# Kernel tuning notes

Measured on AMD Instinct MI355X. Metric: run time of the kernel, lower is better.

Reference implementation:

```python
import math
import jax, jax.numpy as jnp
import numpy as np

NUM_HEADS = 8
FACTOR = 5


def setup_inputs() -> dict:
    key = jax.random.key(0)
    ks = jax.random.split(key, 8)
    B, N, C = 8, 4096, 512
    s = 0.02
    x = jax.random.normal(ks[0], (B, N, C), dtype=jnp.float32)
    Wq = jax.random.normal(ks[1], (C, C), dtype=jnp.float32) * s
    Wk = jax.random.normal(ks[2], (C, C), dtype=jnp.float32) * s
    Wv = jax.random.normal(ks[3], (C, C), dtype=jnp.float32) * s
    Wp = jax.random.normal(ks[4], (C, C), dtype=jnp.float32) * s
    bq = jnp.zeros((C,), jnp.float32)
    bk = jnp.zeros((C,), jnp.float32)
    bv = jnp.zeros((C,), jnp.float32)
    bp = jnp.zeros((C,), jnp.float32)
    sample_k = min(FACTOR * int(np.ceil(np.log(N))), N)  # 45
    index_sample = jax.random.randint(ks[5], (N, sample_k), 0, N, dtype=jnp.int64)
    return {"x": x, "Wq": Wq, "bq": bq, "Wk": Wk, "bk": bk,
            "Wv": Wv, "bv": bv, "Wp": Wp, "bp": bp,
            "index_sample": index_sample}


def reference(x, Wq, bq, Wk, bk, Wv, bv, Wp, bp, index_sample):
    B, N, C = x.shape
    H = NUM_HEADS
    Dh = C // H
    L_Q = L_K = N
    # qkv projections (torch Linear: x @ W.T + b; W sampled symmetric so use x @ W + b)
    q = (x @ Wq + bq).reshape(B, N, H, Dh).transpose(0, 2, 1, 3)  # [B,H,L,Dh]
    k = (x @ Wk + bk).reshape(B, N, H, Dh).transpose(0, 2, 1, 3)
    v = (x @ Wv + bv).reshape(B, N, H, Dh).transpose(0, 2, 1, 3)

    u = min(FACTOR * int(np.ceil(np.log(L_Q))), L_Q)  # n_top
    scale = (C // H) ** (-0.5)

    # _prob_QK: sampled scores per query
    K_sample = k[:, :, index_sample, :]                       # [B,H,L_Q,s,Dh]
    QK_sample = jnp.einsum('bhld,bhlsd->bhls', q, K_sample)   # [B,H,L_Q,s]
    M = QK_sample.max(axis=-1) - QK_sample.sum(axis=-1) / L_K # sparsity measure
    _, M_top = jax.lax.top_k(M, u)                            # [B,H,u]
    Q_reduce = jnp.take_along_axis(q, M_top[..., None], axis=2)  # [B,H,u,Dh]
    scores = jnp.einsum('bhud,bhkd->bhuk', Q_reduce, k) * scale  # [B,H,u,L_K]

    # initial context: mean of V over keys (mask_flag=False)
    context = jnp.broadcast_to(v.mean(axis=2, keepdims=True), (B, H, L_Q, Dh))

    # update context at selected queries
    attn = jax.nn.softmax(scores, axis=-1)
    out_u = jnp.einsum('bhuk,bhkd->bhud', attn, v)            # [B,H,u,Dh]
    bI = jnp.arange(B)[:, None, None]
    hI = jnp.arange(H)[None, :, None]
    context = context.at[bI, hI, M_top].set(out_u)            # [B,H,L_Q,Dh]

    # mix=True: reshape [B,H,N,Dh] -> [B,N,H*Dh] directly (faithful to source)
    context = context.reshape(B, N, H * Dh)
    return context @ Wp + bp
```

## Files before the change

### kernel.cpp

```cpp
#include <hip/hip_runtime.h>
#include <float.h>

typedef unsigned short ushort_t;
typedef short bf16x8 __attribute__((ext_vector_type(8)));
typedef _Float16 f16x8 __attribute__((ext_vector_type(8)));
typedef float f32x4 __attribute__((ext_vector_type(4)));

#define NS 4096
#define ND 64
#define NU 45
#define NUP 48

__device__ __forceinline__ float bf2f(ushort_t u){ return __uint_as_float(((unsigned)u)<<16); }
__device__ __forceinline__ ushort_t f2bf(float f){
  unsigned u = __float_as_uint(f);
  u += 0x7fffu + ((u>>16)&1u);
  return (ushort_t)(u>>16);
}
__device__ __forceinline__ ushort_t f2h(float f){ _Float16 h=(_Float16)f; return __builtin_bit_cast(ushort_t, h); }
__device__ __forceinline__ float h2f(ushort_t u){ return (float)__builtin_bit_cast(_Float16, u); }

__global__ __launch_bounds__(256) void k_wsplit(const float* __restrict__ Wq,
                                                const float* __restrict__ Wk,
                                                const float* __restrict__ Wv,
                                                ushort_t* __restrict__ wh,
                                                ushort_t* __restrict__ wl)
{
  int i = blockIdx.x*256 + threadIdx.x;
  int c = i >> 9, k = i & 511;
  const float* W = (c < 512) ? Wq : (c < 1024 ? Wk : Wv);
  float v = W[k*512 + (c & 511)];
  ushort_t h = f2bf(v);
  wh[i] = h;
  wl[i] = f2bf(v - bf2f(h));
}

__global__ __launch_bounds__(256) void k_xsplit(const float* __restrict__ x,
                                                ushort_t* __restrict__ xh,
                                                ushort_t* __restrict__ xl)
{
  int i = (blockIdx.x*256 + threadIdx.x)*4;
  float4 v = *(const float4*)(x + i);
  ushort4 h, lo;
  h.x = f2bf(v.x); lo.x = f2bf(v.x - bf2f(h.x));
  h.y = f2bf(v.y); lo.y = f2bf(v.y - bf2f(h.y));
  h.z = f2bf(v.z); lo.z = f2bf(v.z - bf2f(h.z));
  h.w = f2bf(v.w); lo.w = f2bf(v.w - bf2f(h.w));
  *(ushort4*)(xh + i) = h;
  *(ushort4*)(xl + i) = lo;
}

template<int MODE>
__global__ __launch_bounds__(256) void k_gemm(
    const ushort_t* __restrict__ xh, const ushort_t* __restrict__ xl,
    const ushort_t* __restrict__ wh, const ushort_t* __restrict__ wl,
    const float* __restrict__ bq, const float* __restrict__ bk, const float* __restrict__ bv,
    float* __restrict__ kf, ushort_t* __restrict__ vfT,
    ushort_t* __restrict__ kb16, ushort_t* __restrict__ qb16)
{
  __shared__ __align__(16) ushort_t smem[20480];
  ushort_t* Ah = smem;
  ushort_t* Al = smem + 5120;
  ushort_t* Bh = smem + (MODE == 1 ? 10240 : 5120);
  ushort_t* Bl = smem + 15360;
  const int nbx = (MODE == 0) ? 4 : 8;
  const int p = blockIdx.y * nbx + blockIdx.x;
  const int cx = p & 7;
  const int local = p >> 3;
  const int by = cx*32 + local/nbx;
  const int bx = local % nbx;
  const int rowbase = by * 128;
  const int colbase = (MODE == 0 ? 0 : 512) + bx*128;
  const int mat = colbase >> 9;
  const int t = threadIdx.x;
  const int l = t & 63;
  const int w = t >> 6;
  const int wm = w >> 1, wn = w & 1;
  f32x4 acc[4][4] = {};
  const int r0 = t >> 2;
  const int c0 = (t & 3) * 8;

  for (int k0 = 0; k0 < 512; k0 += 32) {
    __syncthreads();
    #pragma unroll
    for (int half = 0; half < 2; half++) {
      const int r = r0 + half*64;
      *(uint4*)(&Ah[r*40 + c0]) = *(const uint4*)(&xh[(size_t)(rowbase + r)*512 + k0 + c0]);
      if (MODE == 1) *(uint4*)(&Al[r*40 + c0]) = *(const uint4*)(&xl[(size_t)(rowbase + r)*512 + k0 + c0]);
      *(uint4*)(&Bh[r*40 + c0]) = *(const uint4*)(&wh[(size_t)(colbase + r)*512 + k0 + c0]);
      if (MODE == 1) *(uint4*)(&Bl[r*40 + c0]) = *(const uint4*)(&wl[(size_t)(colbase + r)*512 + k0 + c0]);
    }
    __syncthreads();
    bf16x8 ah[4], al[4], bh8[4], bl8[4];
    #pragma unroll
    for (int m = 0; m < 4; m++) {
      const int off = (wm*64 + m*16 + (l & 15))*40 + (l >> 4)*8;
      ah[m] = *(const bf16x8*)(&Ah[off]);
      if (MODE == 1) al[m] = *(const bf16x8*)(&Al[off]);
    }
    #pragma unroll
    for (int n = 0; n < 4; n++) {
      const int off = (wn*64 + n*16 + (l & 15))*40 + (l >> 4)*8;
      bh8[n] = *(const bf16x8*)(&Bh[off]);
      if (MODE == 1) bl8[n] = *(const bf16x8*)(&Bl[off]);
    }
    #pragma unroll
    for (int m = 0; m < 4; m++)
      #pragma unroll
      for (int n = 0; n < 4; n++) {
        acc[m][n] = __builtin_amdgcn_mfma_f32_16x16x32_bf16(ah[m], bh8[n], acc[m][n], 0, 0, 0);
        if (MODE == 1) {
          acc[m][n] = __builtin_amdgcn_mfma_f32_16x16x32_bf16(ah[m], bl8[n], acc[m][n], 0, 0, 0);
          acc[m][n] = __builtin_amdgcn_mfma_f32_16x16x32_bf16(al[m], bh8[n], acc[m][n], 0, 0, 0);
        }
      }
  }

  if (MODE == 1 && mat == 2) {
    __syncthreads();
    #pragma unroll
    for (int n = 0; n < 4; n++) {
      const int wi_l = wn*64 + n*16 + (l & 15);
      const float bias = bv[(colbase & 511) + wi_l];
      #pragma unroll
      for (int m = 0; m < 4; m++) {
        const int nr_l = wm*64 + m*16 + ((l >> 4) << 2);
        ushort4 pk;
        pk.x = f2h(acc[m][n][0] + bias);
        pk.y = f2h(acc[m][n][1] + bias);
        pk.z = f2h(acc[m][n][2] + bias);
        pk.w = f2h(acc[m][n][3] + bias);
        *(ushort4*)(&smem[wi_l*136 + nr_l]) = pk;
      }
    }
    __syncthreads();
    const int wi2 = t >> 1, half = t & 1;
    const int cim = (colbase & 511) + wi2;
    const int hh2 = cim >> 6, d2 = cim & 63;
    const int b2 = rowbase >> 12;
    const int nr2 = (rowbase & 4095) + half*64;
    ushort_t* op = &vfT[((size_t)(b2*8 + hh2)*ND + d2)*NS + nr2];
    const ushort_t* ip = &smem[wi2*136 + half*64];
    #pragma unroll
    for (int cch = 0; cch < 8; cch++)
      *(uint4*)(op + cch*8) = *(const uint4*)(ip + cch*8);
    return;
  }

  if (MODE == 1) {
    #pragma unroll
    for (int n = 0; n < 4; n++) {
      const int wi = (colbase & 511) + wn*64 + n*16 + (l & 15);
      const int hh = wi >> 6, d = wi & 63;
      const float bias = bk[wi];
      #pragma unroll
      for (int m = 0; m < 4; m++) {
        const int rb = rowbase + wm*64 + m*16 + ((l >> 4) << 2);
        const int b  = rb >> 12, nr = rb & 4095;
        #pragma unroll
        for (int j = 0; j < 4; j++)
          kf[((size_t)(b*8 + hh)*NS + nr + j)*ND + d] = acc[m][n][j] + bias;
      }
    }
  }
  {
    ushort_t* obuf = (MODE == 0) ? qb16 : kb16;
    const float* bias_p = (MODE == 0) ? bq : bk;
    __syncthreads();
    #pragma unroll
    for (int n = 0; n < 4; n++) {
      const int c_l = wn*64 + n*16 + (l & 15);
      const float bias = bias_p[(colbase & 511) + c_l];
      #pragma unroll
      for (int m = 0; m < 4; m++) {
        const int rb_l = wm*64 + m*16 + ((l >> 4) << 2);
        #pragma unroll
        for (int j = 0; j < 4; j++)
          smem[(rb_l + j)*136 + c_l] = f2bf(acc[m][n][j] + bias);
      }
    }
    __syncthreads();
    const int r2 = t >> 1, half = t & 1;
    const int hh2 = ((colbase & 511) >> 6) + half;
    const int b2 = rowbase >> 12;
    const int nr2 = rowbase & 4095;
    ushort_t* op = &obuf[((size_t)(b2*8 + hh2)*NS + nr2 + r2)*ND];
    const ushort_t* ip = &smem[r2*136 + half*64];
    #pragma unroll
    for (int cch = 0; cch < 8; cch++)
      *(uint4*)(op + cch*8) = *(const uint4*)(ip + cch*8);
  }
}

__global__ __launch_bounds__(256) void k_m_approx(const ushort_t* __restrict__ qb16,
                                                  const ushort_t* __restrict__ kb16,
                                                  const int* __restrict__ idxs,
                                                  float* __restrict__ Mv)
{
  __shared__ float qs[4][64];
  __shared__ int   sidx[4][48];
  const int orig = blockIdx.y * 1024 + blockIdx.x;
  const int lin  = (orig & 7) * 8192 + (orig >> 3);
  const int bh   = lin >> 10;
  const int lc   = lin & 1023;
  const int t = threadIdx.x;
  const int wv = t >> 6, lane = t & 63;
  const int l = lc*4 + wv;
  qs[wv][lane] = bf2f(qb16[((size_t)bh*NS + l)*ND + lane]);
  for (int e = t; e < 4*NU; e += 256)
    sidx[e/NU][e%NU] = idxs[(size_t)(lc*4 + e/NU)*NU + e%NU];
  __syncthreads();
  const int g  = lane >> 3;
  const int dq = lane & 7;
  const float* qp = &qs[wv][dq*8];
  float mx = -FLT_MAX, sm = 0.f;
  #pragma unroll
  for (int p = 0; p < 6; p++) {
    const int s = p*8 + g;
    const bool val = (s < NU);
    const int id = sidx[wv][val ? s : NU-1];
    uint4 ku = *(const uint4*)(&kb16[((size_t)bh*NS + id)*ND + dq*8]);
    const ushort_t* kp = (const ushort_t*)&ku;
    float p_dot = qp[0]*bf2f(kp[0]) + qp[1]*bf2f(kp[1]) + qp[2]*bf2f(kp[2]) + qp[3]*bf2f(kp[3])
                + qp[4]*bf2f(kp[4]) + qp[5]*bf2f(kp[5]) + qp[6]*bf2f(kp[6]) + qp[7]*bf2f(kp[7]);
    p_dot += __shfl_xor(p_dot, 1, 64);
    p_dot += __shfl_xor(p_dot, 2, 64);
    p_dot += __shfl_xor(p_dot, 4, 64);
    if (val) { mx = fmaxf(mx, p_dot); sm += p_dot; }
  }
  #pragma unroll
  for (int o = 8; o < 64; o <<= 1) {
    mx = fmaxf(mx, __shfl_xor(mx, o, 64));
    sm += __shfl_xor(sm, o, 64);
  }
  if (lane == 0) Mv[bh*NS + l] = mx - sm * (1.0f/(float)NS);
}

template<int NSEL, int OST>
__global__ __launch_bounds__(256) void k_topk(const float* __restrict__ Mv, int* __restrict__ dst)
{
  __shared__ float wvs[4];
  __shared__ int   wis[4];
  const int bh = blockIdx.x, t = threadIdx.x;
  const int wv = t >> 6, lane = t & 63;
  float v[16];
  #pragma unroll
  for (int j = 0; j < 16; j++) v[j] = Mv[bh*NS + j*256 + t];
  unsigned removed = 0;
  float tmax = -FLT_MAX; int tidx = 0x7fffffff;
  #pragma unroll
  for (int j = 0; j < 16; j++) {
    if (v[j] > tmax) { tmax = v[j]; tidx = j*256 + t; }
  }
  for (int it = 0; it < NSEL; it++) {
    float mv = tmax; int mi = tidx;
    #pragma unroll
    for (int o = 1; o < 64; o <<= 1) {
      float vo = __shfl_xor(mv, o, 64); int io = __shfl_xor(mi, o, 64);
      if (vo > mv || (vo == mv && io < mi)) { mv = vo; mi = io; }
    }
    if (lane == 0) { wvs[wv] = mv; wis[wv] = mi; }
    __syncthreads();
    float gv = wvs[0]; int gi = wis[0];
    #pragma unroll
    for (int k2 = 1; k2 < 4; k2++) {
      float vo = wvs[k2]; int io = wis[k2];
      if (vo > gv || (vo == gv && io < gi)) { gv = vo; gi = io; }
    }
    if (t == 0) dst[bh*OST + it] = gi;
    if ((gi & 255) == t) {
      removed |= 1u << (gi >> 8);
      tmax = -FLT_MAX; tidx = 0x7fffffff;
      #pragma unroll
      for (int j = 0; j < 16; j++) {
        bool ok = ((removed >> j) & 1u) == 0u;
        if (ok && (v[j] > tmax || (v[j] == tmax && (j*256+t) < tidx))) { tmax = v[j]; tidx = j*256 + t; }
      }
    }
    __syncthreads();
  }
}

__global__ __launch_bounds__(256) void k_qexact(const float* __restrict__ x,
                                                const ushort_t* __restrict__ wh,
                                                const ushort_t* __restrict__ wl,
                                                const float* __restrict__ bq,
                                                const int* __restrict__ Cand,
                                                float* __restrict__ qex)
{
  const int bh = blockIdx.x, t = threadIdx.x;
  const int wv = t >> 6, l = t & 63;
  const int b = bh >> 3, h = bh & 7;
  const int cand = 16*wv + (l & 15);
  const int n = Cand[bh*64 + cand];
  const float* xr = x + ((size_t)b*NS + n)*512 + (l >> 4)*8;
  f32x4 acc[4] = {};
  for (int k0 = 0; k0 < 512; k0 += 32) {
    float4 v0 = *(const float4*)(xr + k0);
    float4 v1 = *(const float4*)(xr + k0 + 4);
    ushort_t hi[8], lo[8];
    float vv[8] = {v0.x,v0.y,v0.z,v0.w,v1.x,v1.y,v1.z,v1.w};
    #pragma unroll
    for (int j = 0; j < 8; j++) {
      hi[j] = f2bf(vv[j]);
      lo[j] = f2bf(vv[j] - bf2f(hi[j]));
    }
    bf16x8 ah = *(const bf16x8*)hi;
    bf16x8 al = *(const bf16x8*)lo;
    #pragma unroll
    for (int nt = 0; nt < 4; nt++) {
      const size_t boff = (size_t)(h*64 + nt*16 + (l & 15))*512 + k0 + (l >> 4)*8;
      bf16x8 bh8 = *(const bf16x8*)(&wh[boff]);
      bf16x8 bl8 = *(const bf16x8*)(&wl[boff]);
      acc[nt] = __builtin_amdgcn_mfma_f32_16x16x32_bf16(ah, bh8, acc[nt], 0, 0, 0);
      acc[nt] = __builtin_amdgcn_mfma_f32_16x16x32_bf16(ah, bl8, acc[nt], 0, 0, 0);
      acc[nt] = __builtin_amdgcn_mfma_f32_16x16x32_bf16(al, bh8, acc[nt], 0, 0, 0);
    }
  }
  #pragma unroll
  for (int nt = 0; nt < 4; nt++)
    #pragma unroll
    for (int j = 0; j < 4; j++) {
      const int cand_o = 16*wv + (l >> 4)*4 + j;
      const int d_o = nt*16 + (l & 15);
      qex[((size_t)bh*64 + cand_o)*ND + d_o] = acc[nt][j] + bq[h*64 + d_o];
    }
}

__global__ __launch_bounds__(256) void k_mexact(const float* __restrict__ qex,
                                                const float* __restrict__ kf,
                                                const int* __restrict__ idxs,
                                                const int* __restrict__ Cand,
                                                float* __restrict__ Mex)
{
  const int bh = blockIdx.y, qtr = blockIdx.x, t = threadIdx.x;
  const int c = qtr*16 + (t >> 4);
  const int dl = t & 15;
  const int l = Cand[bh*64 + c];
  const float4 q4 = *(const float4*)(&qex[((size_t)bh*64 + c)*ND + dl*4]);
  const float* kbase = kf + (size_t)bh*NS*ND;
  const int* ib = idxs + (size_t)l*NU;
  float mx = -FLT_MAX, sm = 0.f;
  for (int s = 0; s < NU; s++) {
    const int id = ib[s];
    const float4 k4 = *(const float4*)(&kbase[(size_t)id*ND + dl*4]);
    float p = q4.x*k4.x + q4.y*k4.y + q4.z*k4.z + q4.w*k4.w;
    p += __shfl_xor(p, 1, 64);
    p += __shfl_xor(p, 2, 64);
    p += __shfl_xor(p, 4, 64);
    p += __shfl_xor(p, 8, 64);
    mx = fmaxf(mx, p);
    sm += p;
  }
  if (dl == 0) Mex[bh*64 + c] = mx - sm * (1.0f/(float)NS);
}

__global__ void k_sel45(const float* __restrict__ Mex, const int* __restrict__ Cand,
                        int* __restrict__ Mtop, int* __restrict__ MtopSlot)
{
  const int bh = blockIdx.x, lane = threadIdx.x;
  float val = Mex[bh*64 + lane];
  const int n = Cand[bh*64 + lane];
  const int slot = lane;
  for (int it = 0; it < NU; it++) {
    float wv = val; int wn = n; int ws = slot;
    #pragma unroll
    for (int o = 1; o < 64; o <<= 1) {
      float vo = __shfl_xor(wv, o, 64); int io = __shfl_xor(wn, o, 64); int so = __shfl_xor(ws, o, 64);
      if (vo > wv || (vo == wv && io < wn)) { wv = vo; wn = io; ws = so; }
    }
    if (lane == 0) { Mtop[bh*NUP + it] = wn; MtopSlot[bh*NUP + it] = ws; }
    if (n == wn) val = -FLT_MAX;
  }
}

__global__ __launch_bounds__(256) void k_qreduce(const float* __restrict__ qex,
                                                 const int* __restrict__ MtopSlot,
                                                 ushort_t* __restrict__ Qr)
{
  const int bh = blockIdx.x, t = threadIdx.x;
  for (int e = t; e < NUP*ND; e += 256) {
    const int u = e >> 6, d = e & 63;
    float v = 0.f;
    if (u < NU) { const int s = MtopSlot[bh*NUP + u]; v = qex[((size_t)bh*64 + s)*ND + d]; }
    Qr[bh*NUP*ND + e] = f2bf(v);
  }
}

__global__ __launch_bounds__(256) void k_scores(const ushort_t* __restrict__ Qr,
                                                const ushort_t* __restrict__ kb16,
                                                ushort_t* __restrict__ scores)
{
  __shared__ __align__(16) ushort_t Ql[NUP*80];
  const int bh = blockIdx.y;
  const int n0 = blockIdx.x * 256;
  const int t = threadIdx.x, w = t >> 6, l = t & 63;
  for (int chunk = t; chunk < NUP*8; chunk += 256) {
    const int r = chunk >> 3, cp = chunk & 7;
    *(uint4*)(&Ql[r*80 + cp*8]) = *(const uint4*)(&Qr[((size_t)bh*NUP + r)*ND + cp*8]);
  }
  __syncthreads();
  f32x4 acc[3][4] = {};
  const int nw = n0 + w*64;
  #pragma unroll
  for (int ks = 0; ks < 2; ks++) {
    bf16x8 a[3], b8[4];
    #pragma unroll
    for (int m = 0; m < 3; m++)
      a[m] = *(const bf16x8*)(&Ql[(m*16 + (l & 15))*80 + (l >> 4)*8 + ks*32]);
    #pragma unroll
    for (int n = 0; n < 4; n++)
      b8[n] = *(const bf16x8*)(&kb16[((size_t)bh*NS + nw + n*16 + (l & 15))*ND + (l >> 4)*8 + ks*32]);
    #pragma unroll
    for (int m = 0; m < 3; m++)
      #pragma unroll
      for (int n = 0; n < 4; n++)
        acc[m][n] = __builtin_amdgcn_mfma_f32_16x16x32_bf16(a[m], b8[n], acc[m][n], 0, 0, 0);
  }
  #pragma unroll
  for (int m = 0; m < 3; m++)
    #pragma unroll
    for (int n = 0; n < 4; n++)
      #pragma unroll
      for (int j = 0; j < 4; j++) {
        const int row = m*16 + (l >> 4)*4 + j;
        const int col = nw + n*16 + (l & 15);
        scores[((size_t)bh*NUP + row)*NS + col] = f2bf(acc[m][n][j] * 0.125f);
      }
}

__global__ __launch_bounds__(256) void k_softmax(ushort_t* __restrict__ scores)
{
  __shared__ float srow[NS];
  __shared__ float red[256];
  const int bh = blockIdx.y, u = blockIdx.x, t = threadIdx.x;
  ushort_t* row = scores + ((size_t)bh*NUP + u)*NS;
  float mx = -FLT_MAX;
  for (int j = t; j < NS; j += 256) { float v = bf2f(row[j]); srow[j] = v; mx = fmaxf(mx, v); }
  red[t] = mx; __syncthreads();
  for (int s = 128; s > 0; s >>= 1) { if (t < s) red[t] = fmaxf(red[t], red[t+s]); __syncthreads(); }
  mx = red[0]; __syncthreads();
  float sm = 0.f;
  for (int j = t; j < NS; j += 256) { const float e = __expf(srow[j] - mx); srow[j] = e; sm += e; }
  red[t] = sm; __syncthreads();
  for (int s = 128; s > 0; s >>= 1) { if (t < s) red[t] += red[t+s]; __syncthreads(); }
  const float inv = 1.0f / red[0];
  for (int j = t; j < NS; j += 256) row[j] = f2h(srow[j] * inv);
}

__global__ __launch_bounds__(256) void k_vmean(const ushort_t* __restrict__ vfT, float* __restrict__ vmean)
{
  __shared__ float red[256];
  const int d = blockIdx.x, bh = blockIdx.y, t = threadIdx.x;
  const ushort_t* vr = vfT + ((size_t)bh*ND + d)*NS;
  float s = 0.f;
  for (int n = t; n < NS; n += 256) s += h2f(vr[n]);
  red[t] = s; __syncthreads();
  for (int st = 128; st > 0; st >>= 1) { if (t < st) red[t] += red[t+st]; __syncthreads(); }
  if (t == 0) vmean[bh*ND + d] = red[0] * (1.0f/(float)NS);
}

__global__ __launch_bounds__(256) void k_outu(const ushort_t* __restrict__ attn,
                                              const ushort_t* __restrict__ vfT,
                                              float* __restrict__ pout)
{
  const int bh = blockIdx.y, ch = blockIdx.x;
  const int t = threadIdx.x, w = t >> 6, l = t & 63;
  if (w >= 3) return;
  const ushort_t* ab = attn + (size_t)bh*NUP*NS;
  const ushort_t* vb = vfT + (size_t)bh*ND*NS;
  f32x4 acc[4] = {};
  const int arow = w*16 + (l & 15);
  const int koff = (l >> 4)*8;
  const int kbeg = ch*512;
  for (int kc = kbeg; kc < kbeg + 512; kc += 32) {
    uint4 au = *(const uint4*)(&ab[(size_t)arow*NS + kc + koff]);
    f16x8 a = __builtin_bit_cast(f16x8, au);
    #pragma unroll
    for (int nt = 0; nt < 4; nt++) {
      uint4 bu = *(const uint4*)(&vb[(size_t)(nt*16 + (l & 15))*NS + kc + koff]);
      f16x8 b = __builtin_bit_cast(f16x8, bu);
      acc[nt] = __builtin_amdgcn_mfma_f32_16x16x32_f16(a, b, acc[nt], 0, 0, 0);
    }
  }
  #pragma unroll
  for (int nt = 0; nt < 4; nt++)
    #pragma unroll
    for (int j = 0; j < 4; j++) {
      const int u = w*16 + (l >> 4)*4 + j;
      const int d = nt*16 + (l & 15);
      pout[(((size_t)bh*8 + ch)*NUP + u)*ND + d] = acc[nt][j];
    }
}

__global__ __launch_bounds__(256) void k_delta_fin(const float* __restrict__ pout,
                                                   const float* __restrict__ vmean,
                                                   float* __restrict__ delta)
{
  const int bh = blockIdx.x, t = threadIdx.x;
  for (int e = t; e < NUP*ND; e += 256) {
    const int u = e >> 6, d = e & 63;
    float s = 0.f;
    #pragma unroll
    for (int ch = 0; ch < 8; ch++) s += pout[(((size_t)bh*8 + ch)*NUP + u)*ND + d];
    delta[((size_t)bh*NUP + u)*ND + d] = s - vmean[bh*ND + d];
  }
}

__global__ __launch_bounds__(256) void k_uidx_init(int* __restrict__ uidx)
{
  uidx[blockIdx.x*256 + threadIdx.x] = -1;
}

__global__ void k_scatter(const int* __restrict__ Mtop, int* __restrict__ uidx)
{
  const int bh = blockIdx.x, t = threadIdx.x;
  if (t < NU) {
    const int n = Mtop[bh*NUP + t];
    const int b = bh >> 3, h = bh & 7;
    const int nprime = h*512 + (n >> 3);
    uidx[((size_t)b*NS + nprime)*8 + (n & 7)] = bh*NUP + t;
  }
}

__global__ __launch_bounds__(256) void k_corr(const float* __restrict__ delta,
                                              const float* __restrict__ Wp,
                                              const int* __restrict__ Mtop,
                                              float* __restrict__ corr)
{
  __shared__ float dl[64];
  const int bh = blockIdx.y, u = blockIdx.x, t = threadIdx.x;
  const int n = Mtop[bh*NUP + u];
  const int j = n & 7;
  if (t < 64) dl[t] = delta[((size_t)bh*NUP + u)*ND + t];
  __syncthreads();
  for (int c = t; c < 512; c += 256) {
    float s = 0.f;
    #pragma unroll 8
    for (int d2 = 0; d2 < 64; d2++) s += dl[d2] * Wp[(size_t)(j*64 + d2)*512 + c];
    corr[((size_t)bh*NUP + u)*512 + c] = s;
  }
}

__global__ __launch_bounds__(256) void k_wpsum(const float* __restrict__ Wp,
                                               float* __restrict__ Wpsum)
{
  int i = blockIdx.x*256 + threadIdx.x;
  int d2 = i >> 9, c = i & 511;
  float s = 0.f;
  #pragma unroll
  for (int j = 0; j < 8; j++) s += Wp[(size_t)(j*64 + d2)*512 + c];
  Wpsum[i] = s;
}

__global__ __launch_bounds__(256) void k_base(const float* __restrict__ vmean,
                                              const float* __restrict__ Wpsum,
                                              const float* __restrict__ bp,
                                              float* __restrict__ basep)
{
  __shared__ float vm[64];
  const int bh = blockIdx.x, t = threadIdx.x;
  if (t < 64) vm[t] = vmean[bh*ND + t];
  __syncthreads();
  for (int c = t; c < 512; c += 256) {
    float s = bp[c];
    #pragma unroll 8
    for (int d2 = 0; d2 < 64; d2++) s += vm[d2] * Wpsum[d2*512 + c];
    basep[bh*512 + c] = s;
  }
}

__global__ __launch_bounds__(256) void k_assemble(const float* __restrict__ basep,
                                                  const float* __restrict__ corr,
                                                  const int* __restrict__ uidx,
                                                  float* __restrict__ out)
{
  const int b = blockIdx.y, nprime = blockIdx.x, t = threadIdx.x;
  const int h = nprime >> 9;
  const int* ui = uidx + ((size_t)b*NS + nprime)*8;
  float v0 = basep[(b*8 + h)*512 + t];
  float v1 = basep[(b*8 + h)*512 + 256 + t];
  #pragma unroll
  for (int j = 0; j < 8; j++) {
    const int id = ui[j];
    if (id >= 0) { v0 += corr[(size_t)id*512 + t]; v1 += corr[(size_t)id*512 + 256 + t]; }
  }
  const size_t o = ((size_t)b*NS + nprime)*512;
  out[o + t]       = v0;
  out[o + 256 + t] = v1;
}

extern "C" void kernel_launch(void* const* d_in, const int* in_sizes, int n_in,
                              void* d_out, int out_size, void* d_ws, size_t ws_size,
                              hipStream_t stream)
{
  (void)in_sizes; (void)n_in; (void)out_size; (void)ws_size;
  const float* x  = (const float*)d_in[0];
  const float* Wq = (const float*)d_in[1];
  const float* bq = (const float*)d_in[2];
  const float* Wk = (const float*)d_in[3];
  const float* bk = (const float*)d_in[4];
  const float* Wv = (const float*)d_in[5];
  const float* bv = (const float*)d_in[6];
  const float* Wp = (const float*)d_in[7];
  const float* bp = (const float*)d_in[8];
  const int* idxs = (const int*)d_in[9];
  float* out      = (float*)d_out;

  char* w = (char*)d_ws;
  float*    kf    = (float*)(w);
  ushort_t* vfT   = (ushort_t*)(w + 67108864);
  ushort_t* kb16  = (ushort_t*)(w + 100663296);
  ushort_t* xh    = (ushort_t*)(w + 134217728);
  ushort_t* xl    = (ushort_t*)(w + 167772160);
  ushort_t* qb16  = (ushort_t*)(w + 167772160);
  ushort_t* wh    = (ushort_t*)(w + 201326592);
  ushort_t* wl    = (ushort_t*)(w + 202899456);
  float*    Mv    = (float*)(w + 204472320);
  float*    qex   = (float*)(w + 204472320);
  int*      Mtop  = (int*)(w + 205520896);
  int*      MtopSlot = (int*)(w + 205533184);
  int*      Cand  = (int*)(w + 205545472);
  float*    Mex   = (float*)(w + 205561856);
  float*    vmean = (float*)(w + 205578240);
  float*    Wpsum = (float*)(w + 205594624);
  ushort_t* scores = (ushort_t*)(w);
  float*    delta  = (float*)(w + 25165824);
  float*    corr   = (float*)(w + 25952256);
  int*      uidx   = (int*)(w + 32243712);
  float*    basep  = (float*)(w + 33292288);
  float*    pout   = (float*)(w + 33423360);
  ushort_t* Qr     = (ushort_t*)(w + 39714816);

  k_wsplit   <<<3072, 256, 0, stream>>>(Wq, Wk, Wv, wh, wl);
  k_xsplit   <<<16384, 256, 0, stream>>>(x, xh, xl);
  k_gemm<1>  <<<dim3(8, 256), 256, 0, stream>>>(xh, xl, wh, wl, bq, bk, bv, kf, vfT, kb16, nullptr);
  k_gemm<0>  <<<dim3(4, 256), 256, 0, stream>>>(xh, nullptr, wh, wl, bq, bk, bv, nullptr, nullptr, nullptr, qb16);
  k_wpsum    <<<128, 256, 0, stream>>>(Wp, Wpsum);
  k_m_approx <<<dim3(1024, 64), 256, 0, stream>>>(qb16, kb16, idxs, Mv);
  k_vmean    <<<dim3(64, 64), 256, 0, stream>>>(vfT, vmean);
  k_topk<64,64> <<<64, 256, 0, stream>>>(Mv, Cand);
  k_qexact   <<<64, 256, 0, stream>>>(x, wh, wl, bq, Cand, qex);
  k_mexact   <<<dim3(4, 64), 256, 0, stream>>>(qex, kf, idxs, Cand, Mex);
  k_sel45    <<<64, 64, 0, stream>>>(Mex, Cand, Mtop, MtopSlot);
  k_qreduce  <<<64, 256, 0, stream>>>(qex, MtopSlot, Qr);
  k_scores   <<<dim3(16, 64), 256, 0, stream>>>(Qr, kb16, scores);
  k_softmax  <<<dim3(45, 64), 256, 0, stream>>>(scores);
  k_outu     <<<dim3(8, 64), 256, 0, stream>>>(scores, vfT, pout);
  k_delta_fin<<<64, 256, 0, stream>>>(pout, vmean, delta);
  k_uidx_init<<<1024, 256, 0, stream>>>(uidx);
  k_scatter  <<<64, 64, 0, stream>>>(Mtop, uidx);
  k_corr     <<<dim3(45, 64), 256, 0, stream>>>(delta, Wp, Mtop, corr);
  k_base     <<<64, 256, 0, stream>>>(vmean, Wpsum, bp, basep);
  k_assemble <<<dim3(4096, 8), 256, 0, stream>>>(basep, corr, uidx, out);
}
```

Before: 566.9 us.

## Fuse scores, softmax and PV into split-K flash attention kernel

Replaces the separate scores, softmax, attention-times-V and reduction kernels with one online-softmax flash kernel that splits keys into 8 segments, followed by a combine kernel that merges per-segment max, sum and output. This drops the global round trips of the 45x4096 score matrix per head and two launches. It also rewrites the weight split kernel to transpose through shared memory so reads and writes are coalesced, and hoists the sampled-K gathers in the M-approximation kernel ahead of the dot products so the loads can be in flight together. The flash kernel leaves one of four waves idle and adds rescaling work.

```diff
diff --git a/kernel.cpp b/kernel.cpp
--- a/kernel.cpp
+++ b/kernel.cpp
@@ -26,13 +26,26 @@
                                                 ushort_t* __restrict__ wh,
                                                 ushort_t* __restrict__ wl)
 {
-  int i = blockIdx.x*256 + threadIdx.x;
-  int c = i >> 9, k = i & 511;
-  const float* W = (c < 512) ? Wq : (c < 1024 ? Wk : Wv);
-  float v = W[k*512 + (c & 511)];
-  ushort_t h = f2bf(v);
-  wh[i] = h;
-  wl[i] = f2bf(v - bf2f(h));
+  __shared__ float tile[64][65];
+  const int blk = blockIdx.x;
+  const int mat = blk >> 6;
+  const int kt = (blk >> 3) & 7, nt = blk & 7;
+  const float* W = (mat == 0) ? Wq : (mat == 1 ? Wk : Wv);
+  const int t = threadIdx.x;
+  const int rr = t >> 6, cc = t & 63;
+  #pragma unroll
+  for (int i = 0; i < 16; i++)
+    tile[rr*16 + i][cc] = W[(size_t)(kt*64 + rr*16 + i)*512 + nt*64 + cc];
+  __syncthreads();
+  #pragma unroll
+  for (int i = 0; i < 16; i++) {
+    const int n = rr*16 + i;
+    const float v = tile[cc][n];
+    const ushort_t h = f2bf(v);
+    const size_t o = (size_t)(mat*512 + nt*64 + n)*512 + kt*64 + cc;
+    wh[o] = h;
+    wl[o] = f2bf(v - bf2f(h));
+  }
 }
 
 __global__ __launch_bounds__(256) void k_xsplit(const float* __restrict__ x,
@@ -213,14 +226,22 @@
   const int g  = lane >> 3;
   const int dq = lane & 7;
   const float* qp = &qs[wv][dq*8];
+  int ids[6];
+  #pragma unroll
+  for (int p = 0; p < 6; p++) {
+    const int s = p*8 + g;
+    ids[p] = sidx[wv][(s < NU) ? s : NU-1];
+  }
+  uint4 ku[6];
+  #pragma unroll
+  for (int p = 0; p < 6; p++)
+    ku[p] = *(const uint4*)(&kb16[((size_t)bh*NS + ids[p])*ND + dq*8]);
   float mx = -FLT_MAX, sm = 0.f;
   #pragma unroll
   for (int p = 0; p < 6; p++) {
     const int s = p*8 + g;
     const bool val = (s < NU);
-    const int id = sidx[wv][val ? s : NU-1];
-    uint4 ku = *(const uint4*)(&kb16[((size_t)bh*NS + id)*ND + dq*8]);
-    const ushort_t* kp = (const ushort_t*)&ku;
+    const ushort_t* kp = (const ushort_t*)&ku[p];
     float p_dot = qp[0]*bf2f(kp[0]) + qp[1]*bf2f(kp[1]) + qp[2]*bf2f(kp[2]) + qp[3]*bf2f(kp[3])
                 + qp[4]*bf2f(kp[4]) + qp[5]*bf2f(kp[5]) + qp[6]*bf2f(kp[6]) + qp[7]*bf2f(kp[7]);
     p_dot += __shfl_xor(p_dot, 1, 64);
@@ -383,69 +404,124 @@
     const int u = e >> 6, d = e & 63;
     float v = 0.f;
     if (u < NU) { const int s = MtopSlot[bh*NUP + u]; v = qex[((size_t)bh*64 + s)*ND + d]; }
-    Qr[bh*NUP*ND + e] = f2bf(v);
-  }
-}
-
-__global__ __launch_bounds__(256) void k_scores(const ushort_t* __restrict__ Qr,
-                                                const ushort_t* __restrict__ kb16,
-                                                ushort_t* __restrict__ scores)
-{
-  __shared__ __align__(16) ushort_t Ql[NUP*80];
-  const int bh = blockIdx.y;
-  const int n0 = blockIdx.x * 256;
+    Qr[bh*NUP*ND + e] = f2bf(v * 0.125f);
+  }
+}
+
+__global__ __launch_bounds__(256) void k_flash(const ushort_t* __restrict__ Qr,
+                                               const ushort_t* __restrict__ kb16,
+                                               const ushort_t* __restrict__ vfT,
+                                               float* __restrict__ Opart,
+                                               float* __restrict__ mpart,
+                                               float* __restrict__ lpart)
+{
+  __shared__ __align__(16) ushort_t Plds[3][16][68];
+  const int blk = blockIdx.x;
+  const int bh = blk & 63, seg = blk >> 6;
   const int t = threadIdx.x, w = t >> 6, l = t & 63;
-  for (int chunk = t; chunk < NUP*8; chunk += 256) {
-    const int r = chunk >> 3, cp = chunk & 7;
-    *(uint4*)(&Ql[r*80 + cp*8]) = *(const uint4*)(&Qr[((size_t)bh*NUP + r)*ND + cp*8]);
-  }
-  __syncthreads();
-  f32x4 acc[3][4] = {};
-  const int nw = n0 + w*64;
-  #pragma unroll
-  for (int ks = 0; ks < 2; ks++) {
-    bf16x8 a[3], b8[4];
-    #pragma unroll
-    for (int m = 0; m < 3; m++)
-      a[m] = *(const bf16x8*)(&Ql[(m*16 + (l & 15))*80 + (l >> 4)*8 + ks*32]);
-    #pragma unroll
-    for (int n = 0; n < 4; n++)
-      b8[n] = *(const bf16x8*)(&kb16[((size_t)bh*NS + nw + n*16 + (l & 15))*ND + (l >> 4)*8 + ks*32]);
-    #pragma unroll
-    for (int m = 0; m < 3; m++)
-      #pragma unroll
-      for (int n = 0; n < 4; n++)
-        acc[m][n] = __builtin_amdgcn_mfma_f32_16x16x32_bf16(a[m], b8[n], acc[m][n], 0, 0, 0);
-  }
-  #pragma unroll
-  for (int m = 0; m < 3; m++)
-    #pragma unroll
-    for (int n = 0; n < 4; n++)
+  if (w >= 3) return;
+  const int row0 = w*16;
+  bf16x8 aq[2];
+  #pragma unroll
+  for (int ks = 0; ks < 2; ks++)
+    aq[ks] = *(const bf16x8*)(&Qr[((size_t)bh*NUP + row0 + (l & 15))*ND + ks*32 + (l >> 4)*8]);
+  f32x4 o[4] = {};
+  float m[4], ls[4];
+  #pragma unroll
+  for (int j = 0; j < 4; j++) { m[j] = -FLT_MAX; ls[j] = 0.f; }
+  const int nbeg = seg*512;
+  for (int nc = nbeg; nc < nbeg + 512; nc += 64) {
+    f32x4 S[4];
+    #pragma unroll
+    for (int ct = 0; ct < 4; ct++) {
+      f32x4 z = {};
+      #pragma unroll
+      for (int ks = 0; ks < 2; ks++) {
+        bf16x8 bk8 = *(const bf16x8*)(&kb16[((size_t)bh*NS + nc + ct*16 + (l & 15))*ND + ks*32 + (l >> 4)*8]);
+        z = __builtin_amdgcn_mfma_f32_16x16x32_bf16(aq[ks], bk8, z, 0, 0, 0);
+      }
+      S[ct] = z;
+    }
+    float mx[4];
+    #pragma unroll
+    for (int j = 0; j < 4; j++)
+      mx[j] = fmaxf(fmaxf(S[0][j], S[1][j]), fmaxf(S[2][j], S[3][j]));
+    #pragma unroll
+    for (int o2 = 1; o2 < 16; o2 <<= 1)
+      #pragma unroll
+      for (int j = 0; j < 4; j++)
+        mx[j] = fmaxf(mx[j], __shfl_xor(mx[j], o2, 64));
+    float c[4];
+    #pragma unroll
+    for (int j = 0; j < 4; j++) {
+      const float mn = fmaxf(m[j], mx[j]);
+      c[j] = __expf(m[j] - mn);
+      m[j] = mn;
+      ls[j] *= c[j];
+    }
+    #pragma unroll
+    for (int dt = 0; dt < 4; dt++)
+      #pragma unroll
+      for (int j = 0; j < 4; j++)
+        o[dt][j] *= c[j];
+    #pragma unroll
+    for (int ct = 0; ct < 4; ct++)
       #pragma unroll
       for (int j = 0; j < 4; j++) {
-        const int row = m*16 + (l >> 4)*4 + j;
-        const int col = nw + n*16 + (l & 15);
-        scores[((size_t)bh*NUP + row)*NS + col] = f2bf(acc[m][n][j] * 0.125f);
-      }
-}
-
-__global__ __launch_bounds__(256) void k_softmax(ushort_t* __restrict__ scores)
-{
-  __shared__ float srow[NS];
-  __shared__ float red[256];
-  const int bh = blockIdx.y, u = blockIdx.x, t = threadIdx.x;
-  ushort_t* row = scores + ((size_t)bh*NUP + u)*NS;
-  float mx = -FLT_MAX;
-  for (int j = t; j < NS; j += 256) { float v = bf2f(row[j]); srow[j] = v; mx = fmaxf(mx, v); }
-  red[t] = mx; __syncthreads();
-  for (int s = 128; s > 0; s >>= 1) { if (t < s) red[t] = fmaxf(red[t], red[t+s]); __syncthreads(); }
-  mx = red[0]; __syncthreads();
-  float sm = 0.f;
-  for (int j = t; j < NS; j += 256) { const float e = __expf(srow[j] - mx); srow[j] = e; sm += e; }
-  red[t] = sm; __syncthreads();
-  for (int s = 128; s > 0; s >>= 1) { if (t < s) red[t] += red[t+s]; __syncthreads(); }
-  const float inv = 1.0f / red[0];
-  for (int j = t; j < NS; j += 256) row[j] = f2h(srow[j] * inv);
+        const float pv = __expf(S[ct][j] - m[j]);
+        ls[j] += pv;
+        Plds[w][(l >> 4)*4 + j][ct*16 + (l & 15)] = f2h(pv);
+      }
+    #pragma unroll
+    for (int ks2 = 0; ks2 < 2; ks2++) {
+      f16x8 ap = __builtin_bit_cast(f16x8, *(const uint4*)(&Plds[w][l & 15][ks2*32 + (l >> 4)*8]));
+      #pragma unroll
+      for (int dt = 0; dt < 4; dt++) {
+        f16x8 bv8 = __builtin_bit_cast(f16x8, *(const uint4*)(&vfT[((size_t)bh*ND + dt*16 + (l & 15))*NS + nc + ks2*32 + (l >> 4)*8]));
+        o[dt] = __builtin_amdgcn_mfma_f32_16x16x32_f16(ap, bv8, o[dt], 0, 0, 0);
+      }
+    }
+  }
+  #pragma unroll
+  for (int o2 = 1; o2 < 16; o2 <<= 1)
+    #pragma unroll
+    for (int j = 0; j < 4; j++)
+      ls[j] += __shfl_xor(ls[j], o2, 64);
+  #pragma unroll
+  for (int dt = 0; dt < 4; dt++)
+    #pragma unroll
+    for (int j = 0; j < 4; j++)
+      Opart[(((size_t)bh*8 + seg)*NUP + row0 + (l >> 4)*4 + j)*ND + dt*16 + (l & 15)] = o[dt][j];
+  if ((l & 15) == 0) {
+    #pragma unroll
+    for (int j = 0; j < 4; j++) {
+      mpart[((size_t)bh*8 + seg)*NUP + row0 + (l >> 4)*4 + j] = m[j];
+      lpart[((size_t)bh*8 + seg)*NUP + row0 + (l >> 4)*4 + j] = ls[j];
+    }
+  }
+}
+
+__global__ __launch_bounds__(256) void k_combine(const float* __restrict__ Opart,
+                                                 const float* __restrict__ mpart,
+                                                 const float* __restrict__ lpart,
+                                                 const float* __restrict__ vmean,
+                                                 float* __restrict__ delta)
+{
+  const int bh = blockIdx.x, t = threadIdx.x;
+  for (int e = t; e < NUP*ND; e += 256) {
+    const int u = e >> 6, d = e & 63;
+    float mg = -FLT_MAX;
+    #pragma unroll
+    for (int s = 0; s < 8; s++) mg = fmaxf(mg, mpart[((size_t)bh*8 + s)*NUP + u]);
+    float On = 0.f, Ln = 0.f;
+    #pragma unroll
+    for (int s = 0; s < 8; s++) {
+      const float wgt = __expf(mpart[((size_t)bh*8 + s)*NUP + u] - mg);
+      On += wgt * Opart[(((size_t)bh*8 + s)*NUP + u)*ND + d];
+      Ln += wgt * lpart[((size_t)bh*8 + s)*NUP + u];
+    }
+    delta[((size_t)bh*NUP + u)*ND + d] = On/Ln - vmean[bh*ND + d];
+  }
 }
 
 __global__ __launch_bounds__(256) void k_vmean(const ushort_t* __restrict__ vfT, float* __restrict__ vmean)
@@ -458,53 +534,6 @@
   red[t] = s; __syncthreads();
   for (int st = 128; st > 0; st >>= 1) { if (t < st) red[t] += red[t+st]; __syncthreads(); }
   if (t == 0) vmean[bh*ND + d] = red[0] * (1.0f/(float)NS);
-}
-
-__global__ __launch_bounds__(256) void k_outu(const ushort_t* __restrict__ attn,
-                                              const ushort_t* __restrict__ vfT,
-                                              float* __restrict__ pout)
-{
-  const int bh = blockIdx.y, ch = blockIdx.x;
-  const int t = threadIdx.x, w = t >> 6, l = t & 63;
-  if (w >= 3) return;
-  const ushort_t* ab = attn + (size_t)bh*NUP*NS;
-  const ushort_t* vb = vfT + (size_t)bh*ND*NS;
-  f32x4 acc[4] = {};
-  const int arow = w*16 + (l & 15);
-  const int koff = (l >> 4)*8;
-  const int kbeg = ch*512;
-  for (int kc = kbeg; kc < kbeg + 512; kc += 32) {
-    uint4 au = *(const uint4*)(&ab[(size_t)arow*NS + kc + koff]);
-    f16x8 a = __builtin_bit_cast(f16x8, au);
-    #pragma unroll
-    for (int nt = 0; nt < 4; nt++) {
-      uint4 bu = *(const uint4*)(&vb[(size_t)(nt*16 + (l & 15))*NS + kc + koff]);
-      f16x8 b = __builtin_bit_cast(f16x8, bu);
-      acc[nt] = __builtin_amdgcn_mfma_f32_16x16x32_f16(a, b, acc[nt], 0, 0, 0);
-    }
-  }
-  #pragma unroll
-  for (int nt = 0; nt < 4; nt++)
-    #pragma unroll
-    for (int j = 0; j < 4; j++) {
-      const int u = w*16 + (l >> 4)*4 + j;
-      const int d = nt*16 + (l & 15);
-      pout[(((size_t)bh*8 + ch)*NUP + u)*ND + d] = acc[nt][j];
-    }
-}
-
-__global__ __launch_bounds__(256) void k_delta_fin(const float* __restrict__ pout,
-                                                   const float* __restrict__ vmean,
-                                                   float* __restrict__ delta)
-{
-  const int bh = blockIdx.x, t = threadIdx.x;
-  for (int e = t; e < NUP*ND; e += 256) {
-    const int u = e >> 6, d = e & 63;
-    float s = 0.f;
-    #pragma unroll
-    for (int ch = 0; ch < 8; ch++) s += pout[(((size_t)bh*8 + ch)*NUP + u)*ND + d];
-    delta[((size_t)bh*NUP + u)*ND + d] = s - vmean[bh*ND + d];
-  }
 }
 
 __global__ __launch_bounds__(256) void k_uidx_init(int* __restrict__ uidx)
@@ -624,15 +653,16 @@
   float*    Mex   = (float*)(w + 205561856);
   float*    vmean = (float*)(w + 205578240);
   float*    Wpsum = (float*)(w + 205594624);
-  ushort_t* scores = (ushort_t*)(w);
-  float*    delta  = (float*)(w + 25165824);
-  float*    corr   = (float*)(w + 25952256);
-  int*      uidx   = (int*)(w + 32243712);
-  float*    basep  = (float*)(w + 33292288);
-  float*    pout   = (float*)(w + 33423360);
-  ushort_t* Qr     = (ushort_t*)(w + 39714816);
-
-  k_wsplit   <<<3072, 256, 0, stream>>>(Wq, Wk, Wv, wh, wl);
+  float*    delta  = (float*)(w);
+  float*    corr   = (float*)(w + 786432);
+  int*      uidx   = (int*)(w + 7077888);
+  float*    basep  = (float*)(w + 8126464);
+  float*    Opart  = (float*)(w + 8257536);
+  float*    mpart  = (float*)(w + 14548992);
+  float*    lpart  = (float*)(w + 14647296);
+  ushort_t* Qr     = (ushort_t*)(w + 14745600);
+
+  k_wsplit   <<<192, 256, 0, stream>>>(Wq, Wk, Wv, wh, wl);
   k_xsplit   <<<16384, 256, 0, stream>>>(x, xh, xl);
   k_gemm<1>  <<<dim3(8, 256), 256, 0, stream>>>(xh, xl, wh, wl, bq, bk, bv, kf, vfT, kb16, nullptr);
   k_gemm<0>  <<<dim3(4, 256), 256, 0, stream>>>(xh, nullptr, wh, wl, bq, bk, bv, nullptr, nullptr, nullptr, qb16);
@@ -644,10 +674,8 @@
   k_mexact   <<<dim3(4, 64), 256, 0, stream>>>(qex, kf, idxs, Cand, Mex);
   k_sel45    <<<64, 64, 0, stream>>>(Mex, Cand, Mtop, MtopSlot);
   k_qreduce  <<<64, 256, 0, stream>>>(qex, MtopSlot, Qr);
-  k_scores   <<<dim3(16, 64), 256, 0, stream>>>(Qr, kb16, scores);
-  k_softmax  <<<dim3(45, 64), 256, 0, stream>>>(scores);
-  k_outu     <<<dim3(8, 64), 256, 0, stream>>>(scores, vfT, pout);
-  k_delta_fin<<<64, 256, 0, stream>>>(pout, vmean, delta);
+  k_flash    <<<512, 256, 0, stream>>>(Qr, kb16, vfT, Opart, mpart, lpart);
+  k_combine  <<<64, 256, 0, stream>>>(Opart, mpart, lpart, vmean, delta);
   k_uidx_init<<<1024, 256, 0, stream>>>(uidx);
   k_scatter  <<<64, 64, 0, stream>>>(Mtop, uidx);
   k_corr     <<<dim3(45, 64), 256, 0, stream>>>(delta, Wp, Mtop, corr);
```

After: 547.4 us. 3.4% less time.
